# Performance work log

Hardware: AMD Instinct MI355X
Metric: run time of the kernel (lower is better)

## Reference

```python
import jax, jax.numpy as jnp
import numpy as np

B, C, W, H = 4, 512, 64, 64
DQK = 64


def setup_inputs() -> dict:
    key = jax.random.key(0)
    ks = jax.random.split(key, 8)
    s = 1.0 / np.sqrt(C)
    return {
        "x_s": jax.random.normal(ks[0], (B, C, W, H), jnp.float32),
        "x_t": jax.random.normal(ks[1], (B, C, W, H), jnp.float32),
        "Wq": jax.random.normal(ks[2], (DQK, C), jnp.float32) * s,
        "bq": jnp.zeros((DQK,), jnp.float32),
        "Wk": jax.random.normal(ks[3], (DQK, C), jnp.float32) * s,
        "bk": jnp.zeros((DQK,), jnp.float32),
        "Wv": jax.random.normal(ks[4], (C, C), jnp.float32) * s,
        "bv": jnp.zeros((C,), jnp.float32),
        "gamma": jnp.zeros((1,), jnp.float32),
    }


def reference(x_s, x_t, Wq, bq, Wk, bk, Wv, bv, gamma):
    b, c, w, h = x_t.shape
    n = w * h
    xs = x_s.reshape(b, c, n)  # [B,C,N]
    xt = x_t.reshape(b, c, n)
    # 1x1 convs == channel matmuls
    q = jnp.einsum('dc,bcn->bdn', Wq, xt) + bq[None, :, None]  # [B,64,N]
    k = jnp.einsum('dc,bcn->bdn', Wk, xs) + bk[None, :, None]  # [B,64,N]
    v = jnp.einsum('oc,bcn->bon', Wv, xs) + bv[None, :, None]  # [B,C,N]
    # energy[b,i,j] = <q[:,i], k[:,j]>; softmax over j (keys)
    attn = jax.nn.softmax(jnp.einsum('bdi,bdj->bij', q, k), axis=-1)  # [B,N,N]
    # out = V @ attn^T : out[b,c,i] = sum_j v[b,c,j] * attn[b,i,j]
    out = jnp.einsum('bcj,bij->bci', v, attn).reshape(b, c, w, h)
    return gamma * out + x_s
```

## Files before the change

### kernel.cpp

```cpp
#include <hip/hip_runtime.h>

#define B_ 4
#define C_ 512
#define N_ 4096

typedef __attribute__((ext_vector_type(8))) short short8;
typedef __attribute__((ext_vector_type(4))) short short4v;
typedef __attribute__((ext_vector_type(4))) float float4v;

static __device__ __forceinline__ short bfc(float f) {
  unsigned u = __float_as_uint(f);
  u += 0x7FFFu + ((u >> 16) & 1u);
  return (short)(u >> 16);
}

static __device__ __forceinline__ void bar_lgkm() {
  asm volatile("s_waitcnt lgkmcnt(0)" ::: "memory");
  __builtin_amdgcn_s_barrier();
  asm volatile("" ::: "memory");
}

#define MFMA_BF16 __builtin_amdgcn_mfma_f32_16x16x32_bf16

__global__ __launch_bounds__(256) void wcvt_kernel(
    const float* __restrict__ Wq, const float* __restrict__ Wk,
    const float* __restrict__ Wv,
    short* __restrict__ Wqb, short* __restrict__ Wkb, short* __restrict__ Wvb)
{
  const int i = (blockIdx.x * 256 + threadIdx.x) * 4;
  const float* src; short* dst; int off;
  if (i < 32768)      { src = Wq; dst = Wqb; off = i; }
  else if (i < 65536) { src = Wk; dst = Wkb; off = i - 32768; }
  else                { src = Wv; dst = Wvb; off = i - 65536; }
  float4v v = *(const float4v*)(src + off);
  short4v o;
  o[0] = bfc(v.x); o[1] = bfc(v.y); o[2] = bfc(v.z); o[3] = bfc(v.w);
  *(short4v*)(dst + off) = o;
}

__global__ __launch_bounds__(256, 4) void proj_kernel(
    const float* __restrict__ xs, const float* __restrict__ xt,
    const short* __restrict__ Wqb, const float* __restrict__ bq,
    const short* __restrict__ Wkb, const float* __restrict__ bk,
    const short* __restrict__ Wvb, const float* __restrict__ bv,
    short* __restrict__ Qt, short* __restrict__ Kpk, short* __restrict__ Vpk)
{
  const int bid = blockIdx.x;
  int mode, b, mt, nt;
  const short* W; const float* bias; const float* X;
  if (bid < 256)      { mode = 0; b = bid >> 6;              nt = bid & 63; mt = 0;  W = Wqb; bias = bq; X = xt; }
  else if (bid < 512) { mode = 1; int t = bid - 256; b = t >> 6; nt = t & 63; mt = 0; W = Wkb; bias = bk; X = xs; }
  else                { mode = 2; int t = bid - 512; b = t >> 7; mt = (t >> 6) & 1; nt = t & 63; W = Wvb; bias = bv; X = xs; }

  __shared__ short xlds[2][64][72];

  const int tid  = threadIdx.x;
  const int wave = tid >> 6;
  const int lane = tid & 63;
  const int l15  = lane & 15;
  const int g    = lane >> 4;
  const int n0   = nt * 64;
  const float* xb = X + (size_t)b * C_ * N_;

  const int nloc = tid & 63;
  const int cq   = tid >> 6;

  float v16[16];

#define XLOAD(CS) { \
    const float* xp_ = xb + (size_t)((CS) * 64 + cq * 16) * N_ + n0 + nloc; \
    _Pragma("unroll") \
    for (int i_ = 0; i_ < 16; ++i_) v16[i_] = xp_[(size_t)i_ * N_]; \
  }

#define XWRITE(BUF) { \
    _Pragma("unroll") \
    for (int h_ = 0; h_ < 2; ++h_) { \
      short8 pk_; \
      _Pragma("unroll") \
      for (int j_ = 0; j_ < 8; ++j_) pk_[j_] = bfc(v16[h_ * 8 + j_]); \
      *(short8*)&xlds[BUF][nloc][cq * 16 + h_ * 8] = pk_; \
    } }

  XLOAD(0);
  XWRITE(0);

  if (mode < 2) {
    const int dbase = wave * 16;
    float4v acc[4];
#pragma unroll
    for (int i = 0; i < 4; ++i) acc[i] = (float4v){0.f, 0.f, 0.f, 0.f};

    for (int cs = 0; cs < 8; ++cs) {
      __syncthreads();
      if (cs < 7) XLOAD(cs + 1);
      const int pb = cs & 1;
#pragma unroll
      for (int kk = 0; kk < 2; ++kk) {
        short8 af = *(const short8*)(W + (size_t)(dbase + l15) * C_ + cs * 64 + kk * 32 + g * 8);
#pragma unroll
        for (int ns = 0; ns < 4; ++ns) {
          short8 bf = *(const short8*)&xlds[pb][ns * 16 + l15][kk * 32 + g * 8];
          acc[ns] = MFMA_BF16(af, bf, acc[ns], 0, 0, 0);
        }
      }
      if (cs < 7) XWRITE((cs + 1) & 1);
    }

    float bv4[4];
#pragma unroll
    for (int r = 0; r < 4; ++r) bv4[r] = bias[dbase + g * 4 + r];
#pragma unroll
    for (int ns = 0; ns < 4; ++ns) {
      const int n = n0 + ns * 16 + l15;
      short4v pk;
#pragma unroll
      for (int r = 0; r < 4; ++r) pk[r] = bfc(acc[ns][r] + bv4[r]);
      if (mode == 0)
        *(short4v*)(Qt + ((size_t)b * N_ + n) * 64 + dbase + g * 4) = pk;
      else
        *(short4v*)(Kpk + (((size_t)b * 2 + (dbase >> 5)) * N_ + n) * 32 + (dbase & 31) + g * 4) = pk;
    }
  } else {
    const int dbase = mt * 256 + wave * 64;
    float4v acc[4][4];
#pragma unroll
    for (int i = 0; i < 4; ++i)
#pragma unroll
      for (int j = 0; j < 4; ++j) acc[i][j] = (float4v){0.f, 0.f, 0.f, 0.f};

    for (int cs = 0; cs < 8; ++cs) {
      __syncthreads();
      if (cs < 7) XLOAD(cs + 1);
      const int pb = cs & 1;
#pragma unroll
      for (int kk = 0; kk < 2; ++kk) {
        short8 af[4];
#pragma unroll
        for (int dt = 0; dt < 4; ++dt)
          af[dt] = *(const short8*)(W + (size_t)(dbase + dt * 16 + l15) * C_ + cs * 64 + kk * 32 + g * 8);
#pragma unroll
        for (int ns = 0; ns < 4; ++ns) {
          short8 bf = *(const short8*)&xlds[pb][ns * 16 + l15][kk * 32 + g * 8];
#pragma unroll
          for (int dt = 0; dt < 4; ++dt)
            acc[dt][ns] = MFMA_BF16(af[dt], bf, acc[dt][ns], 0, 0, 0);
        }
      }
      if (cs < 7) XWRITE((cs + 1) & 1);
    }

#pragma unroll
    for (int dt = 0; dt < 4; ++dt) {
      float bv4[4];
#pragma unroll
      for (int r = 0; r < 4; ++r) bv4[r] = bias[dbase + dt * 16 + g * 4 + r];
#pragma unroll
      for (int ns = 0; ns < 4; ++ns) {
        const int n = n0 + ns * 16 + l15;
        const int jt = n >> 5, jr = n & 31;
        short* vp = Vpk + (((size_t)b * 128 + jt) * 512 + dbase + dt * 16 + g * 4) * 32 + jr;
#pragma unroll
        for (int r = 0; r < 4; ++r) vp[(size_t)r * 32] = bfc(acc[dt][ns][r] + bv4[r]);
      }
    }
  }
#undef XLOAD
#undef XWRITE
}

__global__ __launch_bounds__(512, 4) void flash_kernel(
    const short* __restrict__ Qt, const short* __restrict__ Kpk, const short* __restrict__ Vpk,
    const float* __restrict__ xs, const float* __restrict__ gp, float* __restrict__ out)
{
  const int bid = blockIdx.x;
  const int xcd = bid & 7, slot = bid >> 3;
  const int b     = xcd >> 1;
  const int chalf = xcd & 1;
  const int q0    = slot * 64;

  __shared__ float S_lds[64][68];
  __shared__ short P_lds[64][72];
  __shared__ float l_sm[64];

  const int tid = threadIdx.x;
  const int wave = tid >> 6, lane = tid & 63;
  const int l15 = lane & 15, g = lane >> 4;

  const int s_rt  = wave >> 1;
  const int s_ct0 = (wave & 1) * 2;
  const int cb    = chalf * 256 + wave * 32;

  short8 qf0, qf1;
  {
    const short* qp = Qt + ((size_t)b * N_ + q0 + s_rt * 16 + l15) * 64 + g * 8;
    qf0 = *(const short8*)qp;
    qf1 = *(const short8*)(qp + 32);
  }

  float4v acc[4][2];
#pragma unroll
  for (int i = 0; i < 4; ++i)
#pragma unroll
    for (int j = 0; j < 2; ++j) acc[i][j] = (float4v){0.f,0.f,0.f,0.f};

  float lsum = 0.f;
  const int srow = tid >> 3, ssub = tid & 7;

  const short* kbase  = Kpk + ((size_t)b * 2 * N_ + s_ct0 * 16 + l15) * 32 + g * 8;
  const short* vbaseA = Vpk + ((size_t)(b * 128) * 512 + cb + l15) * 32 + g * 8;
  const short* vbaseB = vbaseA + (size_t)16 * 32;

#define VLOAD(V00, V01, V10, V11, JT0) { \
    const size_t off_ = (size_t)(JT0) * (512 * 32); \
    V00 = *(const short8*)(vbaseA + off_); \
    V01 = *(const short8*)(vbaseB + off_); \
    V10 = *(const short8*)(vbaseA + off_ + 512 * 32); \
    V11 = *(const short8*)(vbaseB + off_ + 512 * 32); \
  }

#define KLOAD(K00, K01, K10, K11, J0) { \
    const short* kp_ = kbase + (size_t)(J0) * 32; \
    K00 = *(const short8*)kp_; \
    K01 = *(const short8*)(kp_ + (size_t)N_ * 32); \
    K10 = *(const short8*)(kp_ + 16 * 32); \
    K11 = *(const short8*)(kp_ + 16 * 32 + (size_t)N_ * 32); \
  }

#define STEP(KC00, KC01, KC10, KC11, VC00, VC01, VC10, VC11, \
             KN00, KN01, KN10, KN11, VN00, VN01, VN10, VN11, JS) { \
    const int jn_ = ((JS) + 1) & 63; \
    VLOAD(VN00, VN01, VN10, VN11, jn_ * 2)     \
    KLOAD(KN00, KN01, KN10, KN11, jn_ * 64)    \
    _Pragma("unroll") \
    for (int t_ = 0; t_ < 2; ++t_) { \
      float4v s_ = (float4v){0.f, 0.f, 0.f, 0.f}; \
      s_ = MFMA_BF16(qf0, t_ ? KC10 : KC00, s_, 0, 0, 0); \
      s_ = MFMA_BF16(qf1, t_ ? KC11 : KC01, s_, 0, 0, 0); \
      _Pragma("unroll") \
      for (int r_ = 0; r_ < 4; ++r_) \
        S_lds[s_rt * 16 + g * 4 + r_][(s_ct0 + t_) * 16 + l15] = s_[r_]; \
    } \
    bar_lgkm(); \
    { \
      float4v s0_ = *(const float4v*)&S_lds[srow][ssub * 8]; \
      float4v s1_ = *(const float4v*)&S_lds[srow][ssub * 8 + 4]; \
      float p_[8]; \
      p_[0]=__expf(s0_.x-20.f); p_[1]=__expf(s0_.y-20.f); p_[2]=__expf(s0_.z-20.f); p_[3]=__expf(s0_.w-20.f); \
      p_[4]=__expf(s1_.x-20.f); p_[5]=__expf(s1_.y-20.f); p_[6]=__expf(s1_.z-20.f); p_[7]=__expf(s1_.w-20.f); \
      short8 pk_; \
      _Pragma("unroll") \
      for (int r_ = 0; r_ < 8; ++r_) pk_[r_] = bfc(p_[r_]); \
      *(short8*)&P_lds[srow][ssub * 8] = pk_; \
      lsum += p_[0]+p_[1]+p_[2]+p_[3]+p_[4]+p_[5]+p_[6]+p_[7]; \
    } \
    bar_lgkm(); \
    { \
      __builtin_amdgcn_s_setprio(1); \
      _Pragma("unroll") \
      for (int kt_ = 0; kt_ < 2; ++kt_) { \
        short8 pa_[4]; \
        _Pragma("unroll") \
        for (int rt_ = 0; rt_ < 4; ++rt_) \
          pa_[rt_] = *(const short8*)&P_lds[rt_ * 16 + l15][kt_ * 32 + g * 8]; \
        const short8 vb0_ = kt_ ? VC10 : VC00; \
        const short8 vb1_ = kt_ ? VC11 : VC01; \
        _Pragma("unroll") \
        for (int rt_ = 0; rt_ < 4; ++rt_) { \
          acc[rt_][0] = MFMA_BF16(pa_[rt_], vb0_, acc[rt_][0], 0, 0, 0); \
          acc[rt_][1] = MFMA_BF16(pa_[rt_], vb1_, acc[rt_][1], 0, 0, 0); \
        } \
      } \
      __builtin_amdgcn_s_setprio(0); \
    } \
  }

  short8 ka0, ka1, ka2, ka3, kb0, kb1, kb2, kb3;
  short8 va0, va1, va2, va3, vb0v, vb1v, vb2v, vb3v;
  KLOAD(ka0, ka1, ka2, ka3, 0)
  VLOAD(va0, va1, va2, va3, 0)

  for (int js = 0; js < 64; js += 2) {
    STEP(ka0, ka1, ka2, ka3, va0, va1, va2, va3,
         kb0, kb1, kb2, kb3, vb0v, vb1v, vb2v, vb3v, js)
    STEP(kb0, kb1, kb2, kb3, vb0v, vb1v, vb2v, vb3v,
         ka0, ka1, ka2, ka3, va0, va1, va2, va3, js + 1)
  }
#undef STEP
#undef KLOAD
#undef VLOAD

  lsum += __shfl_xor(lsum, 1);
  lsum += __shfl_xor(lsum, 2);
  lsum += __shfl_xor(lsum, 4);
  if ((tid & 7) == 0) l_sm[srow] = lsum;
  __syncthreads();

  const float gm = gp[0];
  float sc[4][4];
#pragma unroll
  for (int rt = 0; rt < 4; ++rt) {
    float4v lv = *(const float4v*)&l_sm[rt * 16 + g * 4];
#pragma unroll
    for (int r = 0; r < 4; ++r) sc[rt][r] = gm / lv[r];
  }
#pragma unroll
  for (int rt = 0; rt < 4; ++rt)
#pragma unroll
    for (int ct = 0; ct < 2; ++ct) {
      const int c = cb + ct * 16 + l15;
      const size_t base = ((size_t)b * C_ + c) * N_ + q0 + rt * 16 + g * 4;
      float4v xv = *(const float4v*)(xs + base);
      float4v o;
#pragma unroll
      for (int r = 0; r < 4; ++r) o[r] = acc[rt][ct][r] * sc[rt][r] + xv[r];
      *(float4v*)(out + base) = o;
    }
}

extern "C" void kernel_launch(void* const* d_in, const int* in_sizes, int n_in,
                              void* d_out, int out_size, void* d_ws, size_t ws_size,
                              hipStream_t stream) {
  const float* xs = (const float*)d_in[0];
  const float* xt = (const float*)d_in[1];
  const float* Wq = (const float*)d_in[2];
  const float* bq = (const float*)d_in[3];
  const float* Wk = (const float*)d_in[4];
  const float* bk = (const float*)d_in[5];
  const float* Wv = (const float*)d_in[6];
  const float* bv = (const float*)d_in[7];
  const float* gm = (const float*)d_in[8];
  float* out = (float*)d_out;

  char* ws = (char*)d_ws;
  short* Qt  = (short*)(ws);
  short* Kpk = (short*)(ws + (size_t)(2 << 20));
  short* Vpk = (short*)(ws + (size_t)(4 << 20));
  short* Wqb = (short*)(ws + (size_t)(20 << 20));
  short* Wkb = (short*)(ws + (size_t)(20 << 20) + 65536);
  short* Wvb = (short*)(ws + (size_t)(20 << 20) + 131072);

  hipLaunchKernelGGL(wcvt_kernel, dim3(320), dim3(256), 0, stream,
                     Wq, Wk, Wv, Wqb, Wkb, Wvb);
  hipLaunchKernelGGL(proj_kernel, dim3(1024), dim3(256), 0, stream,
                     xs, xt, Wqb, bq, Wkb, bk, Wvb, bv, Qt, Kpk, Vpk);
  hipLaunchKernelGGL(flash_kernel, dim3(512), dim3(512), 0, stream,
                     Qt, Kpk, Vpk, xs, gm, out);
}
```

Measured before the change: 273.7 us.

## Pre-transpose inputs to bf16, compute S transposed in registers, double-buffer P

A new prep kernel converts x_s and x_t to bf16 in an N-major transposed layout, alongside the weight conversion. The projection kernel then reads its MFMA operands directly from global memory instead of staging through LDS, and Q and K projections share one 512-thread block. The flash kernel computes S transposed (K as A operand) so each wave exponentiates its own MFMA output and writes P straight to a double-buffered LDS tile. This removes the S round trip through LDS and one barrier per step. The cost is an extra full pass that writes 32MB of transposed bf16 activations, plus global-memory operand loads in the projection with no LDS reuse.

Measured after the change: 351.6 us. 28.4% more time.

```diff
diff --git a/kernel.cpp b/kernel.cpp
--- a/kernel.cpp
+++ b/kernel.cpp
@@ -22,142 +22,132 @@
 
 #define MFMA_BF16 __builtin_amdgcn_mfma_f32_16x16x32_bf16
 
-__global__ __launch_bounds__(256) void wcvt_kernel(
+__global__ __launch_bounds__(256) void prep_kernel(
+    const float* __restrict__ xs, const float* __restrict__ xt,
     const float* __restrict__ Wq, const float* __restrict__ Wk,
     const float* __restrict__ Wv,
+    short* __restrict__ xTs, short* __restrict__ xTt,
     short* __restrict__ Wqb, short* __restrict__ Wkb, short* __restrict__ Wvb)
 {
-  const int i = (blockIdx.x * 256 + threadIdx.x) * 4;
-  const float* src; short* dst; int off;
-  if (i < 32768)      { src = Wq; dst = Wqb; off = i; }
-  else if (i < 65536) { src = Wk; dst = Wkb; off = i - 32768; }
-  else                { src = Wv; dst = Wvb; off = i - 65536; }
-  float4v v = *(const float4v*)(src + off);
-  short4v o;
-  o[0] = bfc(v.x); o[1] = bfc(v.y); o[2] = bfc(v.z); o[3] = bfc(v.w);
-  *(short4v*)(dst + off) = o;
-}
-
-__global__ __launch_bounds__(256, 4) void proj_kernel(
-    const float* __restrict__ xs, const float* __restrict__ xt,
+  const int bid = blockIdx.x;
+  const int tid = threadIdx.x;
+  if (bid < 4096) {
+    __shared__ short lds[64][72];
+    const int t2 = bid & 2047;
+    const int bb = t2 >> 9, ct = (t2 >> 6) & 7, nt = t2 & 63;
+    const float* src = (bid < 2048) ? xs : xt;
+    short* dst = (bid < 2048) ? xTs : xTt;
+    const int c0 = ct * 64, n0 = nt * 64;
+    const int cr = tid >> 4;
+    const int nq = (tid & 15) * 4;
+#pragma unroll
+    for (int p = 0; p < 4; ++p) {
+      const int c = c0 + p * 16 + cr;
+      float4v v = *(const float4v*)(src + (size_t)(bb * C_ + c) * N_ + n0 + nq);
+      lds[nq + 0][p * 16 + cr] = bfc(v.x);
+      lds[nq + 1][p * 16 + cr] = bfc(v.y);
+      lds[nq + 2][p * 16 + cr] = bfc(v.z);
+      lds[nq + 3][p * 16 + cr] = bfc(v.w);
+    }
+    __syncthreads();
+    const int n = tid >> 2, q = tid & 3;
+    short8 a  = *(const short8*)&lds[n][q * 16];
+    short8 b2 = *(const short8*)&lds[n][q * 16 + 8];
+    short* dp = dst + (size_t)(bb * N_ + n0 + n) * C_ + c0 + q * 16;
+    *(short8*)dp = a;
+    *(short8*)(dp + 8) = b2;
+  } else {
+    const int i = (bid - 4096) * 1024 + tid * 4;
+    const float* src; short* dstw; int off;
+    if (i < 32768)      { src = Wq; dstw = Wqb; off = i; }
+    else if (i < 65536) { src = Wk; dstw = Wkb; off = i - 32768; }
+    else                { src = Wv; dstw = Wvb; off = i - 65536; }
+    float4v v = *(const float4v*)(src + off);
+    short4v o;
+    o[0] = bfc(v.x); o[1] = bfc(v.y); o[2] = bfc(v.z); o[3] = bfc(v.w);
+    *(short4v*)(dstw + off) = o;
+  }
+}
+
+__global__ __launch_bounds__(512, 4) void proj_kernel(
+    const short* __restrict__ xTs, const short* __restrict__ xTt,
     const short* __restrict__ Wqb, const float* __restrict__ bq,
     const short* __restrict__ Wkb, const float* __restrict__ bk,
     const short* __restrict__ Wvb, const float* __restrict__ bv,
-    short* __restrict__ Qt, short* __restrict__ Kpk, short* __restrict__ Vpk)
+    short* __restrict__ Qpk, short* __restrict__ Kt, short* __restrict__ Vpk)
 {
   const int bid = blockIdx.x;
-  int mode, b, mt, nt;
-  const short* W; const float* bias; const float* X;
-  if (bid < 256)      { mode = 0; b = bid >> 6;              nt = bid & 63; mt = 0;  W = Wqb; bias = bq; X = xt; }
-  else if (bid < 512) { mode = 1; int t = bid - 256; b = t >> 6; nt = t & 63; mt = 0; W = Wkb; bias = bk; X = xs; }
-  else                { mode = 2; int t = bid - 512; b = t >> 7; mt = (t >> 6) & 1; nt = t & 63; W = Wvb; bias = bv; X = xs; }
-
-  __shared__ short xlds[2][64][72];
-
-  const int tid  = threadIdx.x;
-  const int wave = tid >> 6;
-  const int lane = tid & 63;
-  const int l15  = lane & 15;
-  const int g    = lane >> 4;
-  const int n0   = nt * 64;
-  const float* xb = X + (size_t)b * C_ * N_;
-
-  const int nloc = tid & 63;
-  const int cq   = tid >> 6;
-
-  float v16[16];
-
-#define XLOAD(CS) { \
-    const float* xp_ = xb + (size_t)((CS) * 64 + cq * 16) * N_ + n0 + nloc; \
-    _Pragma("unroll") \
-    for (int i_ = 0; i_ < 16; ++i_) v16[i_] = xp_[(size_t)i_ * N_]; \
-  }
-
-#define XWRITE(BUF) { \
-    _Pragma("unroll") \
-    for (int h_ = 0; h_ < 2; ++h_) { \
-      short8 pk_; \
-      _Pragma("unroll") \
-      for (int j_ = 0; j_ < 8; ++j_) pk_[j_] = bfc(v16[h_ * 8 + j_]); \
-      *(short8*)&xlds[BUF][nloc][cq * 16 + h_ * 8] = pk_; \
-    } }
-
-  XLOAD(0);
-  XWRITE(0);
-
-  if (mode < 2) {
-    const int dbase = wave * 16;
+  const int tid = threadIdx.x;
+  const int wave = tid >> 6, lane = tid & 63;
+  const int l15 = lane & 15, g = lane >> 4;
+
+  if (bid < 256) {
+    const int b = bid >> 6, nt = bid & 63;
+    const int isK = wave >> 2;
+    const int dbase = (wave & 3) * 16;
+    const short* W = isK ? Wkb : Wqb;
+    const float* bias = isK ? bk : bq;
+    const short* X = isK ? xTs : xTt;
+    const short* xrow = X + (size_t)(b * N_ + nt * 64) * C_;
     float4v acc[4];
 #pragma unroll
     for (int i = 0; i < 4; ++i) acc[i] = (float4v){0.f, 0.f, 0.f, 0.f};
-
-    for (int cs = 0; cs < 8; ++cs) {
-      __syncthreads();
-      if (cs < 7) XLOAD(cs + 1);
-      const int pb = cs & 1;
-#pragma unroll
-      for (int kk = 0; kk < 2; ++kk) {
-        short8 af = *(const short8*)(W + (size_t)(dbase + l15) * C_ + cs * 64 + kk * 32 + g * 8);
-#pragma unroll
-        for (int ns = 0; ns < 4; ++ns) {
-          short8 bf = *(const short8*)&xlds[pb][ns * 16 + l15][kk * 32 + g * 8];
-          acc[ns] = MFMA_BF16(af, bf, acc[ns], 0, 0, 0);
-        }
+    const short* wp = W + (size_t)(dbase + l15) * C_ + g * 8;
+#pragma unroll 2
+    for (int kk = 0; kk < 16; ++kk) {
+      short8 af = *(const short8*)(wp + kk * 32);
+#pragma unroll
+      for (int ns = 0; ns < 4; ++ns) {
+        short8 bf = *(const short8*)(xrow + (size_t)(ns * 16 + l15) * C_ + kk * 32 + g * 8);
+        acc[ns] = MFMA_BF16(af, bf, acc[ns], 0, 0, 0);
       }
-      if (cs < 7) XWRITE((cs + 1) & 1);
-    }
-
+    }
     float bv4[4];
 #pragma unroll
     for (int r = 0; r < 4; ++r) bv4[r] = bias[dbase + g * 4 + r];
 #pragma unroll
     for (int ns = 0; ns < 4; ++ns) {
-      const int n = n0 + ns * 16 + l15;
+      const int n = nt * 64 + ns * 16 + l15;
       short4v pk;
 #pragma unroll
       for (int r = 0; r < 4; ++r) pk[r] = bfc(acc[ns][r] + bv4[r]);
-      if (mode == 0)
-        *(short4v*)(Qt + ((size_t)b * N_ + n) * 64 + dbase + g * 4) = pk;
+      if (isK)
+        *(short4v*)(Kt + ((size_t)b * N_ + n) * 64 + dbase + g * 4) = pk;
       else
-        *(short4v*)(Kpk + (((size_t)b * 2 + (dbase >> 5)) * N_ + n) * 32 + (dbase & 31) + g * 4) = pk;
+        *(short4v*)(Qpk + (((size_t)b * 2 + (dbase >> 5)) * N_ + n) * 32 + (dbase & 31) + g * 4) = pk;
     }
   } else {
-    const int dbase = mt * 256 + wave * 64;
+    const int t = bid - 256;
+    const int b = t >> 6, nt = t & 63;
+    const int dbase = wave * 64;
+    const short* xrow = xTs + (size_t)(b * N_ + nt * 64) * C_;
     float4v acc[4][4];
 #pragma unroll
     for (int i = 0; i < 4; ++i)
 #pragma unroll
       for (int j = 0; j < 4; ++j) acc[i][j] = (float4v){0.f, 0.f, 0.f, 0.f};
-
-    for (int cs = 0; cs < 8; ++cs) {
-      __syncthreads();
-      if (cs < 7) XLOAD(cs + 1);
-      const int pb = cs & 1;
-#pragma unroll
-      for (int kk = 0; kk < 2; ++kk) {
-        short8 af[4];
+#pragma unroll 2
+    for (int kk = 0; kk < 16; ++kk) {
+      short8 af[4];
+#pragma unroll
+      for (int dt = 0; dt < 4; ++dt)
+        af[dt] = *(const short8*)(Wvb + (size_t)(dbase + dt * 16 + l15) * C_ + kk * 32 + g * 8);
+#pragma unroll
+      for (int ns = 0; ns < 4; ++ns) {
+        short8 bf = *(const short8*)(xrow + (size_t)(ns * 16 + l15) * C_ + kk * 32 + g * 8);
 #pragma unroll
         for (int dt = 0; dt < 4; ++dt)
-          af[dt] = *(const short8*)(W + (size_t)(dbase + dt * 16 + l15) * C_ + cs * 64 + kk * 32 + g * 8);
-#pragma unroll
-        for (int ns = 0; ns < 4; ++ns) {
-          short8 bf = *(const short8*)&xlds[pb][ns * 16 + l15][kk * 32 + g * 8];
-#pragma unroll
-          for (int dt = 0; dt < 4; ++dt)
-            acc[dt][ns] = MFMA_BF16(af[dt], bf, acc[dt][ns], 0, 0, 0);
-        }
+          acc[dt][ns] = MFMA_BF16(af[dt], bf, acc[dt][ns], 0, 0, 0);
       }
-      if (cs < 7) XWRITE((cs + 1) & 1);
-    }
-
+    }
 #pragma unroll
     for (int dt = 0; dt < 4; ++dt) {
       float bv4[4];
 #pragma unroll
-      for (int r = 0; r < 4; ++r) bv4[r] = bias[dbase + dt * 16 + g * 4 + r];
+      for (int r = 0; r < 4; ++r) bv4[r] = bv[dbase + dt * 16 + g * 4 + r];
 #pragma unroll
       for (int ns = 0; ns < 4; ++ns) {
-        const int n = n0 + ns * 16 + l15;
+        const int n = nt * 64 + ns * 16 + l15;
         const int jt = n >> 5, jr = n & 31;
         short* vp = Vpk + (((size_t)b * 128 + jt) * 512 + dbase + dt * 16 + g * 4) * 32 + jr;
 #pragma unroll
@@ -165,135 +155,135 @@
       }
     }
   }
-#undef XLOAD
-#undef XWRITE
 }
 
 __global__ __launch_bounds__(512, 4) void flash_kernel(
-    const short* __restrict__ Qt, const short* __restrict__ Kpk, const short* __restrict__ Vpk,
-    const float* __restrict__ xs, const float* __restrict__ gp, float* __restrict__ out)
+    const short* __restrict__ Qpk, const short* __restrict__ Kt,
+    const short* __restrict__ Vpk,
+    const float* __restrict__ xs, const float* __restrict__ gp,
+    float* __restrict__ out)
 {
   const int bid = blockIdx.x;
   const int xcd = bid & 7, slot = bid >> 3;
-  const int b     = xcd >> 1;
-  const int chalf = xcd & 1;
-  const int q0    = slot * 64;
-
-  __shared__ float S_lds[64][68];
-  __shared__ short P_lds[64][72];
+  const int b = xcd >> 1, chalf = xcd & 1;
+  const int q0 = slot * 64;
+
+  __shared__ short P_lds[2][64][72];
+  __shared__ float l_part[8][16];
   __shared__ float l_sm[64];
 
   const int tid = threadIdx.x;
   const int wave = tid >> 6, lane = tid & 63;
   const int l15 = lane & 15, g = lane >> 4;
-
-  const int s_rt  = wave >> 1;
-  const int s_ct0 = (wave & 1) * 2;
-  const int cb    = chalf * 256 + wave * 32;
-
-  short8 qf0, qf1;
+  const int it = wave >> 1, jt2 = wave & 1;
+  const int cb = chalf * 256 + wave * 32;
+  const int prow = it * 16 + l15;
+
+  short8 qB0, qB1;
   {
-    const short* qp = Qt + ((size_t)b * N_ + q0 + s_rt * 16 + l15) * 64 + g * 8;
-    qf0 = *(const short8*)qp;
-    qf1 = *(const short8*)(qp + 32);
-  }
+    const short* qp = Qpk + ((size_t)(b * 2) * N_ + q0 + prow) * 32 + g * 8;
+    qB0 = *(const short8*)qp;
+    qB1 = *(const short8*)(qp + (size_t)N_ * 32);
+  }
+
+  const short* kbase = Kt + ((size_t)b * N_ + jt2 * 32 + l15) * 64 + g * 8;
+  const short* vbase = Vpk + ((size_t)(b * 128) * 512 + cb + l15) * 32 + g * 8;
 
   float4v acc[4][2];
 #pragma unroll
   for (int i = 0; i < 4; ++i)
 #pragma unroll
     for (int j = 0; j < 2; ++j) acc[i][j] = (float4v){0.f,0.f,0.f,0.f};
-
   float lsum = 0.f;
-  const int srow = tid >> 3, ssub = tid & 7;
-
-  const short* kbase  = Kpk + ((size_t)b * 2 * N_ + s_ct0 * 16 + l15) * 32 + g * 8;
-  const short* vbaseA = Vpk + ((size_t)(b * 128) * 512 + cb + l15) * 32 + g * 8;
-  const short* vbaseB = vbaseA + (size_t)16 * 32;
-
-#define VLOAD(V00, V01, V10, V11, JT0) { \
-    const size_t off_ = (size_t)(JT0) * (512 * 32); \
-    V00 = *(const short8*)(vbaseA + off_); \
-    V01 = *(const short8*)(vbaseB + off_); \
-    V10 = *(const short8*)(vbaseA + off_ + 512 * 32); \
-    V11 = *(const short8*)(vbaseB + off_ + 512 * 32); \
-  }
-
-#define KLOAD(K00, K01, K10, K11, J0) { \
-    const short* kp_ = kbase + (size_t)(J0) * 32; \
-    K00 = *(const short8*)kp_; \
-    K01 = *(const short8*)(kp_ + (size_t)N_ * 32); \
-    K10 = *(const short8*)(kp_ + 16 * 32); \
-    K11 = *(const short8*)(kp_ + 16 * 32 + (size_t)N_ * 32); \
-  }
-
-#define STEP(KC00, KC01, KC10, KC11, VC00, VC01, VC10, VC11, \
-             KN00, KN01, KN10, KN11, VN00, VN01, VN10, VN11, JS) { \
-    const int jn_ = ((JS) + 1) & 63; \
-    VLOAD(VN00, VN01, VN10, VN11, jn_ * 2)     \
-    KLOAD(KN00, KN01, KN10, KN11, jn_ * 64)    \
+
+#define KLOADA(D0, D1, D2, D3, J) { \
+    const short* kp_ = kbase + (size_t)(J) * 4096; \
+    D0 = *(const short8*)(kp_);               \
+    D1 = *(const short8*)(kp_ + 32);          \
+    D2 = *(const short8*)(kp_ + 1024);        \
+    D3 = *(const short8*)(kp_ + 1024 + 32);   \
+  }
+
+#define VLOADM(D0, D1, D2, D3, JT) { \
+    const short* vp_ = vbase + (size_t)(JT) * (512 * 32); \
+    D0 = *(const short8*)(vp_);                     \
+    D1 = *(const short8*)(vp_ + 16 * 32);           \
+    D2 = *(const short8*)(vp_ + 512 * 32);          \
+    D3 = *(const short8*)(vp_ + 512 * 32 + 16 * 32);\
+  }
+
+#define QKEXP(NXT, K0, K1, K2, K3) { \
+    float4v s0_ = (float4v){0.f,0.f,0.f,0.f}; \
+    float4v s1_ = (float4v){0.f,0.f,0.f,0.f}; \
+    s0_ = MFMA_BF16(K0, qB0, s0_, 0, 0, 0); \
+    s0_ = MFMA_BF16(K1, qB1, s0_, 0, 0, 0); \
+    s1_ = MFMA_BF16(K2, qB0, s1_, 0, 0, 0); \
+    s1_ = MFMA_BF16(K3, qB1, s1_, 0, 0, 0); \
+    float p_[8]; \
+    p_[0]=__expf(s0_.x-20.f); p_[1]=__expf(s0_.y-20.f); \
+    p_[2]=__expf(s0_.z-20.f); p_[3]=__expf(s0_.w-20.f); \
+    p_[4]=__expf(s1_.x-20.f); p_[5]=__expf(s1_.y-20.f); \
+    p_[6]=__expf(s1_.z-20.f); p_[7]=__expf(s1_.w-20.f); \
+    short4v pk0_, pk1_; \
     _Pragma("unroll") \
-    for (int t_ = 0; t_ < 2; ++t_) { \
-      float4v s_ = (float4v){0.f, 0.f, 0.f, 0.f}; \
-      s_ = MFMA_BF16(qf0, t_ ? KC10 : KC00, s_, 0, 0, 0); \
-      s_ = MFMA_BF16(qf1, t_ ? KC11 : KC01, s_, 0, 0, 0); \
-      _Pragma("unroll") \
-      for (int r_ = 0; r_ < 4; ++r_) \
-        S_lds[s_rt * 16 + g * 4 + r_][(s_ct0 + t_) * 16 + l15] = s_[r_]; \
+    for (int r_ = 0; r_ < 4; ++r_) { pk0_[r_] = bfc(p_[r_]); pk1_[r_] = bfc(p_[4 + r_]); } \
+    *(short4v*)&P_lds[NXT][prow][jt2 * 32 + g * 4] = pk0_; \
+    *(short4v*)&P_lds[NXT][prow][jt2 * 32 + 16 + g * 4] = pk1_; \
+    lsum += (p_[0]+p_[1]) + (p_[2]+p_[3]) + (p_[4]+p_[5]) + (p_[6]+p_[7]); \
+  }
+
+#define PVSTEP(CUR, V0, V1, V2, V3) { \
+    __builtin_amdgcn_s_setprio(1); \
+    _Pragma("unroll") \
+    for (int rt_ = 0; rt_ < 4; ++rt_) { \
+      short8 pa_ = *(const short8*)&P_lds[CUR][rt_ * 16 + l15][g * 8]; \
+      acc[rt_][0] = MFMA_BF16(pa_, V0, acc[rt_][0], 0, 0, 0); \
+      acc[rt_][1] = MFMA_BF16(pa_, V1, acc[rt_][1], 0, 0, 0); \
     } \
+    _Pragma("unroll") \
+    for (int rt_ = 0; rt_ < 4; ++rt_) { \
+      short8 pb_ = *(const short8*)&P_lds[CUR][rt_ * 16 + l15][32 + g * 8]; \
+      acc[rt_][0] = MFMA_BF16(pb_, V2, acc[rt_][0], 0, 0, 0); \
+      acc[rt_][1] = MFMA_BF16(pb_, V3, acc[rt_][1], 0, 0, 0); \
+    } \
+    __builtin_amdgcn_s_setprio(0); \
+  }
+
+#define STEP(S, VU0, VU1, VU2, VU3, VF0, VF1, VF2, VF3) { \
+    KLOADA(kc0, kc1, kc2, kc3, ((S) + 1) & 63) \
+    VLOADM(VF0, VF1, VF2, VF3, (((S) + 1) & 63) * 2) \
+    PVSTEP((S) & 1, VU0, VU1, VU2, VU3) \
+    QKEXP(((S) + 1) & 1, kc0, kc1, kc2, kc3) \
     bar_lgkm(); \
-    { \
-      float4v s0_ = *(const float4v*)&S_lds[srow][ssub * 8]; \
-      float4v s1_ = *(const float4v*)&S_lds[srow][ssub * 8 + 4]; \
-      float p_[8]; \
-      p_[0]=__expf(s0_.x-20.f); p_[1]=__expf(s0_.y-20.f); p_[2]=__expf(s0_.z-20.f); p_[3]=__expf(s0_.w-20.f); \
-      p_[4]=__expf(s1_.x-20.f); p_[5]=__expf(s1_.y-20.f); p_[6]=__expf(s1_.z-20.f); p_[7]=__expf(s1_.w-20.f); \
-      short8 pk_; \
-      _Pragma("unroll") \
-      for (int r_ = 0; r_ < 8; ++r_) pk_[r_] = bfc(p_[r_]); \
-      *(short8*)&P_lds[srow][ssub * 8] = pk_; \
-      lsum += p_[0]+p_[1]+p_[2]+p_[3]+p_[4]+p_[5]+p_[6]+p_[7]; \
-    } \
-    bar_lgkm(); \
-    { \
-      __builtin_amdgcn_s_setprio(1); \
-      _Pragma("unroll") \
-      for (int kt_ = 0; kt_ < 2; ++kt_) { \
-        short8 pa_[4]; \
-        _Pragma("unroll") \
-        for (int rt_ = 0; rt_ < 4; ++rt_) \
-          pa_[rt_] = *(const short8*)&P_lds[rt_ * 16 + l15][kt_ * 32 + g * 8]; \
-        const short8 vb0_ = kt_ ? VC10 : VC00; \
-        const short8 vb1_ = kt_ ? VC11 : VC01; \
-        _Pragma("unroll") \
-        for (int rt_ = 0; rt_ < 4; ++rt_) { \
-          acc[rt_][0] = MFMA_BF16(pa_[rt_], vb0_, acc[rt_][0], 0, 0, 0); \
-          acc[rt_][1] = MFMA_BF16(pa_[rt_], vb1_, acc[rt_][1], 0, 0, 0); \
-        } \
-      } \
-      __builtin_amdgcn_s_setprio(0); \
-    } \
-  }
-
-  short8 ka0, ka1, ka2, ka3, kb0, kb1, kb2, kb3;
-  short8 va0, va1, va2, va3, vb0v, vb1v, vb2v, vb3v;
-  KLOAD(ka0, ka1, ka2, ka3, 0)
-  VLOAD(va0, va1, va2, va3, 0)
-
-  for (int js = 0; js < 64; js += 2) {
-    STEP(ka0, ka1, ka2, ka3, va0, va1, va2, va3,
-         kb0, kb1, kb2, kb3, vb0v, vb1v, vb2v, vb3v, js)
-    STEP(kb0, kb1, kb2, kb3, vb0v, vb1v, vb2v, vb3v,
-         ka0, ka1, ka2, ka3, va0, va1, va2, va3, js + 1)
-  }
+  }
+
+  short8 kc0, kc1, kc2, kc3;
+  short8 va0, va1, va2, va3, vb0, vb1, vb2, vb3;
+
+  KLOADA(kc0, kc1, kc2, kc3, 0)
+  VLOADM(va0, va1, va2, va3, 0)
+  QKEXP(0, kc0, kc1, kc2, kc3)
+  bar_lgkm();
+
+  for (int s = 0; s < 62; s += 2) {
+    STEP(s,     va0, va1, va2, va3, vb0, vb1, vb2, vb3)
+    STEP(s + 1, vb0, vb1, vb2, vb3, va0, va1, va2, va3)
+  }
+  STEP(62, va0, va1, va2, va3, vb0, vb1, vb2, vb3)
+  PVSTEP(1, vb0, vb1, vb2, vb3)
+
 #undef STEP
-#undef KLOAD
-#undef VLOAD
-
-  lsum += __shfl_xor(lsum, 1);
-  lsum += __shfl_xor(lsum, 2);
-  lsum += __shfl_xor(lsum, 4);
-  if ((tid & 7) == 0) l_sm[srow] = lsum;
+#undef PVSTEP
+#undef QKEXP
+#undef VLOADM
+#undef KLOADA
+
+  lsum += __shfl_xor(lsum, 16);
+  lsum += __shfl_xor(lsum, 32);
+  if (lane < 16) l_part[wave][lane] = lsum;
+  __syncthreads();
+  if (tid < 64)
+    l_sm[tid] = l_part[(tid >> 4) * 2][tid & 15] + l_part[(tid >> 4) * 2 + 1][tid & 15];
   __syncthreads();
 
   const float gm = gp[0];
@@ -333,17 +323,19 @@
   float* out = (float*)d_out;
 
   char* ws = (char*)d_ws;
-  short* Qt  = (short*)(ws);
-  short* Kpk = (short*)(ws + (size_t)(2 << 20));
-  short* Vpk = (short*)(ws + (size_t)(4 << 20));
-  short* Wqb = (short*)(ws + (size_t)(20 << 20));
-  short* Wkb = (short*)(ws + (size_t)(20 << 20) + 65536);
-  short* Wvb = (short*)(ws + (size_t)(20 << 20) + 131072);
-
-  hipLaunchKernelGGL(wcvt_kernel, dim3(320), dim3(256), 0, stream,
-                     Wq, Wk, Wv, Wqb, Wkb, Wvb);
-  hipLaunchKernelGGL(proj_kernel, dim3(1024), dim3(256), 0, stream,
-                     xs, xt, Wqb, bq, Wkb, bk, Wvb, bv, Qt, Kpk, Vpk);
+  short* xTs = (short*)(ws);
+  short* xTt = (short*)(ws + (size_t)(16 << 20));
+  short* Vpk = (short*)(ws + (size_t)(32 << 20));
+  short* Qpk = (short*)(ws + (size_t)(48 << 20));
+  short* Kt  = (short*)(ws + (size_t)(50 << 20));
+  short* Wqb = (short*)(ws + (size_t)(52 << 20));
+  short* Wkb = (short*)(ws + (size_t)(52 << 20) + 65536);
+  short* Wvb = (short*)(ws + (size_t)(52 << 20) + 131072);
+
+  hipLaunchKernelGGL(prep_kernel, dim3(4416), dim3(256), 0, stream,
+                     xs, xt, Wq, Wk, Wv, xTs, xTt, Wqb, Wkb, Wvb);
+  hipLaunchKernelGGL(proj_kernel, dim3(512), dim3(512), 0, stream,
+                     xTs, xTt, Wqb, bq, Wkb, bk, Wvb, bv, Qpk, Kt, Vpk);
   hipLaunchKernelGGL(flash_kernel, dim3(512), dim3(512), 0, stream,
-                     Qt, Kpk, Vpk, xs, gm, out);
-}
+                     Qpk, Kt, Vpk, xs, gm, out);
+}
```
